# Kernel tuning notes

Hardware: AMD Instinct MI355X
Metric: run time of the kernel (lower is better)

Reference implementation:

```python
import jax, jax.numpy as jnp
import numpy as np

D_MODEL = 1024
NUM_HEADS = 16
D_K = D_MODEL // NUM_HEADS
B, T = 2, 2048
NEG = -1e9


def setup_inputs() -> dict:
    key = jax.random.key(0)
    ks = jax.random.split(key, 12)
    s = 1.0 / np.sqrt(D_MODEL)
    q = jax.random.normal(ks[0], (B, T, D_MODEL), jnp.float32)
    k = jax.random.normal(ks[1], (B, T, D_MODEL), jnp.float32)
    v = jax.random.normal(ks[2], (B, T, D_MODEL), jnp.float32)
    # padding mask: True = valid key; realistic per-example lengths
    lengths = jnp.array([T, 3 * T // 4], dtype=jnp.int32)
    key_padding_mask = jnp.arange(T)[None, :] < lengths[:, None]
    Wq = jax.random.uniform(ks[3], (D_MODEL, D_MODEL), jnp.float32, -s, s)
    bq = jax.random.uniform(ks[4], (D_MODEL,), jnp.float32, -s, s)
    Wk = jax.random.uniform(ks[5], (D_MODEL, D_MODEL), jnp.float32, -s, s)
    bk = jax.random.uniform(ks[6], (D_MODEL,), jnp.float32, -s, s)
    Wv = jax.random.uniform(ks[7], (D_MODEL, D_MODEL), jnp.float32, -s, s)
    bv = jax.random.uniform(ks[8], (D_MODEL,), jnp.float32, -s, s)
    Wo = jax.random.uniform(ks[9], (D_MODEL, D_MODEL), jnp.float32, -s, s)
    bo = jax.random.uniform(ks[10], (D_MODEL,), jnp.float32, -s, s)
    return {"q": q, "k": k, "v": v, "key_padding_mask": key_padding_mask,
            "Wq": Wq, "bq": bq, "Wk": Wk, "bk": bk,
            "Wv": Wv, "bv": bv, "Wo": Wo, "bo": bo}


def reference(q, k, v, key_padding_mask, Wq, bq, Wk, bk, Wv, bv, Wo, bo):
    Bq, Tq, D = q.shape
    Tk = k.shape[1]
    # projections (torch Linear: x @ W.T + b), split heads -> [B, H, T, d_k]
    Q = (q @ Wq.T + bq).reshape(Bq, Tq, NUM_HEADS, D_K).transpose(0, 2, 1, 3)
    K = (k @ Wk.T + bk).reshape(Bq, Tk, NUM_HEADS, D_K).transpose(0, 2, 1, 3)
    V = (v @ Wv.T + bv).reshape(Bq, Tk, NUM_HEADS, D_K).transpose(0, 2, 1, 3)
    logits = jnp.einsum("bhqd,bhkd->bhqk", Q, K) / jnp.sqrt(jnp.float32(D_K))
    causal = jnp.tril(jnp.ones((Tq, Tk), dtype=bool))  # [Tq, Tk]
    mask = causal[None, None, :, :] & key_padding_mask[:, None, None, :]
    logits = jnp.where(mask, logits, NEG)
    scores = jax.nn.softmax(logits, axis=-1)
    out = jnp.einsum("bhqk,bhkd->bhqd", scores, V)
    out = out.transpose(0, 2, 1, 3).reshape(Bq, Tq, D)
    # dropout is identity in eval mode
    return out @ Wo.T + bo
```

## Files before the change

### kernel.cpp

```cpp
#include <hip/hip_runtime.h>
#include <stdint.h>

#define D_MODEL 1024
#define NHEAD 16
#define DK 64
#define BATCH 2
#define SEQ 2048
#define NROW 4096

typedef __attribute__((ext_vector_type(8))) _Float16 f16x8;
typedef __attribute__((ext_vector_type(4))) float f32x4;

__device__ __forceinline__ uint16_t f2h(float x) {
    _Float16 h = (_Float16)x;
    union { _Float16 h; uint16_t u; } cv;
    cv.h = h;
    return cv.u;
}

__device__ __forceinline__ float fexp2(float x) {
#if __has_builtin(__builtin_amdgcn_exp2f)
    return __builtin_amdgcn_exp2f(x);
#else
    return exp2f(x);
#endif
}

__device__ __forceinline__ void lds_dma16(const uint16_t* g, uint16_t* l) {
    __builtin_amdgcn_global_load_lds((const __attribute__((address_space(1))) void*)g,
                                     (__attribute__((address_space(3))) void*)l,
                                     16, 0, 0);
}

struct CvtArgs {
    const float* src[7];
    uint16_t* dst[7];
    int n4[7];
};
__global__ void cvt_all_kernel(CvtArgs a, const int* __restrict__ mask, int* __restrict__ lens_ctr) {
    int t = blockIdx.y;
    if (t == 7) {
        if (blockIdx.x != 0) return;
        __shared__ int red[256];
        int tid = threadIdx.x;
        int mx = 0;
        for (int i = tid; i < 1024; i += 256) { int v = mask[i]; if (v > mx) mx = v; }
        red[tid] = mx; __syncthreads();
        for (int s = 128; s > 0; s >>= 1) { if (tid < s) { if (red[tid+s] > red[tid]) red[tid] = red[tid+s]; } __syncthreads(); }
        int bytemode = (red[0] > 1);
        __syncthreads();
        const unsigned char* mb = (const unsigned char*)mask;
        for (int b = 0; b < BATCH; ++b) {
            int cnt = 0;
            for (int tt = tid; tt < SEQ; tt += 256) {
                int v = bytemode ? (int)mb[b*SEQ + tt] : mask[b*SEQ + tt];
                cnt += (v != 0) ? 1 : 0;
            }
            red[tid] = cnt; __syncthreads();
            for (int s = 128; s > 0; s >>= 1) { if (tid < s) red[tid] += red[tid+s]; __syncthreads(); }
            if (tid == 0) lens_ctr[b] = red[0];
            __syncthreads();
        }
        if (tid == 0) lens_ctr[2] = 0;
        return;
    }
    const float* src = a.src[t];
    uint16_t* dst = a.dst[t];
    int n4 = a.n4[t];
    int i = blockIdx.x * blockDim.x + threadIdx.x;
    int stride = gridDim.x * blockDim.x;
    for (; i < n4; i += stride) {
        float4 v = ((const float4*)src)[i];
        ushort4 o;
        o.x = f2h(v.x); o.y = f2h(v.y); o.z = f2h(v.z); o.w = f2h(v.w);
        ((ushort4*)dst)[i] = o;
    }
}

__device__ __forceinline__ void gemm_tile_core(const uint16_t* __restrict__ A,
                                               const uint16_t* __restrict__ W,
                                               int bx, int by,
                                               uint16_t* As, uint16_t* Bs,
                                               f32x4 (&acc)[4][4]) {
    const f32x4 fzero = {0.f, 0.f, 0.f, 0.f};
    int tid = threadIdx.x;
    int lane = tid & 63, wave = tid >> 6;
    int wm = wave >> 1, wn = wave & 1;
    int l15 = lane & 15, quad = lane >> 4;
    int rl = lane >> 3, cb8 = lane & 7;
#pragma unroll
    for (int mi = 0; mi < 4; mi++)
#pragma unroll
        for (int ni = 0; ni < 4; ni++) acc[mi][ni] = fzero;

    for (int k0 = 0; k0 < D_MODEL; k0 += 64) {
        __syncthreads();
#pragma unroll
        for (int i = 0; i < 4; ++i) {
            int d8 = wave * 4 + i;
            int row = d8 * 8 + rl;
            int cbg = cb8 ^ rl;
            lds_dma16(A + (size_t)(bx * 128 + row) * D_MODEL + k0 + cbg * 8, As + d8 * 512);
            lds_dma16(W + (size_t)(by * 128 + row) * D_MODEL + k0 + cbg * 8, Bs + d8 * 512);
        }
        __syncthreads();
#pragma unroll
        for (int ks = 0; ks < 2; ks++) {
            f16x8 af[4], bf[4];
#pragma unroll
            for (int mi = 0; mi < 4; mi++) {
                int row = wm * 64 + mi * 16 + l15;
                af[mi] = *(const f16x8*)(As + row * 64 + (((ks * 4 + quad) ^ (row & 7)) * 8));
            }
#pragma unroll
            for (int ni = 0; ni < 4; ni++) {
                int row = wn * 64 + ni * 16 + l15;
                bf[ni] = *(const f16x8*)(Bs + row * 64 + (((ks * 4 + quad) ^ (row & 7)) * 8));
            }
#pragma unroll
            for (int mi = 0; mi < 4; mi++)
#pragma unroll
                for (int ni = 0; ni < 4; ni++)
                    acc[mi][ni] = __builtin_amdgcn_mfma_f32_16x16x32_f16(af[mi], bf[ni], acc[mi][ni], 0, 0, 0);
        }
    }
}

#define TS_STRIDE 136
__global__ __launch_bounds__(256, 3) void qkv_kernel(
    const uint16_t* __restrict__ qb, const uint16_t* __restrict__ kb, const uint16_t* __restrict__ vb,
    const uint16_t* __restrict__ wq, const uint16_t* __restrict__ wk, const uint16_t* __restrict__ wv,
    const float* __restrict__ bq, const float* __restrict__ bk, const float* __restrict__ bv,
    uint16_t* __restrict__ Qh, uint16_t* __restrict__ Kh, uint16_t* __restrict__ Vth) {
    __shared__ uint16_t smem[TS_STRIDE * 128];
    uint16_t* As = smem;
    uint16_t* Bs = smem + 128 * 64;
    int v = blockIdx.z;
    const uint16_t* A = (v == 0) ? qb : ((v == 1) ? kb : vb);
    const uint16_t* W = (v == 0) ? wq : ((v == 1) ? wk : wv);
    const float* bias = (v == 0) ? bq : ((v == 1) ? bk : bv);
    f32x4 acc[4][4];
    gemm_tile_core(A, W, blockIdx.x, blockIdx.y, As, Bs, acc);

    int tid = threadIdx.x, lane = tid & 63, wave = tid >> 6;
    int wm = wave >> 1, wn = wave & 1, l15 = lane & 15, quad = lane >> 4;
    const float QSCALE = 0.125f * 1.44269504088896f;

    if (v == 2) {
        __syncthreads();
        uint16_t* Ts = smem;
#pragma unroll
        for (int mi = 0; mi < 4; mi++) {
#pragma unroll
            for (int ni = 0; ni < 4; ni++) {
                int col = wn * 64 + ni * 16 + l15;
                float bcol = bias[blockIdx.y * 128 + col];
#pragma unroll
                for (int r = 0; r < 4; r++) {
                    int tl = wm * 64 + mi * 16 + quad * 4 + r;
                    Ts[col * TS_STRIDE + tl] = f2h(acc[mi][ni][r] + bcol);
                }
            }
        }
        __syncthreads();
        int col = tid >> 1, th = (tid & 1) << 6;
        int gcol = blockIdx.y * 128 + col;
        int h = gcol >> 6, d = gcol & 63;
        int grow0 = blockIdx.x * 128;
        int b = grow0 >> 11, t = (grow0 & (SEQ - 1)) + th;
        size_t base = (((size_t)(b * NHEAD + h) << 6) + d) * SEQ + t;
#pragma unroll
        for (int j = 0; j < 8; j++)
            *(uint4*)(Vth + base + j * 8) = *(const uint4*)(Ts + col * TS_STRIDE + th + j * 8);
        return;
    }

#pragma unroll
    for (int mi = 0; mi < 4; mi++) {
#pragma unroll
        for (int ni = 0; ni < 4; ni++) {
            int gcol = blockIdx.y * 128 + wn * 64 + ni * 16 + l15;
            float bcol = bias[gcol];
            int h = gcol >> 6, d = gcol & 63;
#pragma unroll
            for (int r = 0; r < 4; r++) {
                int grow = blockIdx.x * 128 + wm * 64 + mi * 16 + quad * 4 + r;
                int b = grow >> 11, t = grow & (SEQ - 1);
                float val = acc[mi][ni][r] + bcol;
                size_t bh = (size_t)(b * NHEAD + h);
                if (v == 0) Qh[(bh * SEQ + t) * 64 + d] = f2h(val * QSCALE);
                else        Kh[(bh * SEQ + t) * 64 + d] = f2h(val);
            }
        }
    }
}

__global__ __launch_bounds__(256, 3) void outproj_kernel(
    const uint16_t* __restrict__ attn, const uint16_t* __restrict__ wo,
    const float* __restrict__ bo, float* __restrict__ out) {
    __shared__ uint16_t As[128 * 64], Bs[128 * 64];
    f32x4 acc[4][4];
    gemm_tile_core(attn, wo, blockIdx.x, blockIdx.y, As, Bs, acc);
    int tid = threadIdx.x, lane = tid & 63, wave = tid >> 6;
    int wm = wave >> 1, wn = wave & 1, l15 = lane & 15, quad = lane >> 4;
#pragma unroll
    for (int mi = 0; mi < 4; mi++) {
#pragma unroll
        for (int ni = 0; ni < 4; ni++) {
            int gcol = blockIdx.y * 128 + wn * 64 + ni * 16 + l15;
            float bcol = bo[gcol];
#pragma unroll
            for (int r = 0; r < 4; r++) {
                int grow = blockIdx.x * 128 + wm * 64 + mi * 16 + quad * 4 + r;
                out[(size_t)grow * D_MODEL + gcol] = acc[mi][ni][r] + bcol;
            }
        }
    }
}

__device__ __forceinline__ void flash_one(
    int qt, int bh, int b, int h, int L,
    const uint16_t* __restrict__ Qh, const uint16_t* __restrict__ Kh, const uint16_t* __restrict__ Vth,
    uint16_t* __restrict__ attn,
    uint16_t* Kt0, uint16_t* Kt1, uint16_t* Vt0, uint16_t* Vt1, uint16_t* Ptw) {
    const f32x4 fzero = {0.f, 0.f, 0.f, 0.f};
    const float MFIX = 6.0f;
    int tid = threadIdx.x, lane = tid & 63, w = tid >> 6;
    int l15 = lane & 15, quad = lane >> 4, l7 = l15 & 7;
    int q0 = qt * 64;
    int rl = lane >> 3, cb8 = lane & 7;

    f16x8 ones;
#pragma unroll
    for (int j = 0; j < 8; j++) ones[j] = (_Float16)1.0f;

    f16x8 qf[2];
#pragma unroll
    for (int ks = 0; ks < 2; ks++)
        qf[ks] = *(const f16x8*)(Qh + ((size_t)bh * SEQ + q0 + w * 16 + l15) * 64 + ks * 32 + quad * 8);

    f32x4 o_acc[4], l_acc = fzero;
#pragma unroll
    for (int ni = 0; ni < 4; ni++) o_acc[ni] = fzero;

    int nkt_p = (L + 63) >> 6;
    int nkt = (qt + 1 < nkt_p) ? (qt + 1) : nkt_p;

    uint16_t* Ktb[2] = {Kt0, Kt1};
    uint16_t* Vtb[2] = {Vt0, Vt1};

    auto stage = [&](int kt_, int buf_) {
#pragma unroll
        for (int i_ = 0; i_ < 2; ++i_) {
            int d8 = w * 2 + i_;
            int row = d8 * 8 + rl;
            int cbg = cb8 ^ rl;
            lds_dma16(Kh + ((size_t)bh * SEQ + kt_ * 64 + row) * 64 + cbg * 8, Ktb[buf_] + d8 * 512);
            lds_dma16(Vth + (((size_t)bh << 6) + row) * SEQ + kt_ * 64 + cbg * 8, Vtb[buf_] + d8 * 512);
        }
    };

    stage(0, 0);
    __syncthreads();

    for (int kt = 0; kt < nkt; ++kt) {
        int cur = kt & 1;
        if (kt + 1 < nkt) stage(kt + 1, cur ^ 1);

        f32x4 s_acc[4];
#pragma unroll
        for (int ni = 0; ni < 4; ni++) s_acc[ni] = fzero;
#pragma unroll
        for (int ks = 0; ks < 2; ks++) {
            f16x8 kf[4];
#pragma unroll
            for (int ni = 0; ni < 4; ni++)
                kf[ni] = *(const f16x8*)(Ktb[cur] + (ni * 16 + l15) * 64 + ((ks * 4 + quad) ^ l7) * 8);
#pragma unroll
            for (int ni = 0; ni < 4; ni++)
                s_acc[ni] = __builtin_amdgcn_mfma_f32_16x16x32_f16(qf[ks], kf[ni], s_acc[ni], 0, 0, 0);
        }

        bool full = (kt < qt) && (kt * 64 + 64 <= L);
#pragma unroll
        for (int r = 0; r < 4; r++) {
            int prow = quad * 4 + r;
            int q_idx = q0 + w * 16 + prow;
            int pr7 = prow & 7;
#pragma unroll
            for (int ni = 0; ni < 4; ni++) {
                float s = s_acc[ni][r];
                if (!full) {
                    int key = kt * 64 + ni * 16 + l15;
                    s = ((key <= q_idx) && (key < L)) ? s : -1e9f;
                }
                float p = fexp2(s - MFIX);
                int cb = ni * 2 + (l15 >> 3);
                Ptw[prow * 64 + ((cb ^ pr7) * 8) + l7] = f2h(p);
            }
        }
        __asm__ __volatile__("" ::: "memory");

#pragma unroll
        for (int ks = 0; ks < 2; ks++) {
            f16x8 pa = *(const f16x8*)(Ptw + l15 * 64 + (((ks * 4 + quad) ^ l7) * 8));
            l_acc = __builtin_amdgcn_mfma_f32_16x16x32_f16(pa, ones, l_acc, 0, 0, 0);
            f16x8 vbf[4];
#pragma unroll
            for (int ni = 0; ni < 4; ni++)
                vbf[ni] = *(const f16x8*)(Vtb[cur] + (ni * 16 + l15) * 64 + ((ks * 4 + quad) ^ l7) * 8);
#pragma unroll
            for (int ni = 0; ni < 4; ni++)
                o_acc[ni] = __builtin_amdgcn_mfma_f32_16x16x32_f16(pa, vbf[ni], o_acc[ni], 0, 0, 0);
        }
        __syncthreads();
    }

#pragma unroll
    for (int r = 0; r < 4; r++) {
        float inv = 1.0f / l_acc[r];
        int q_idx = q0 + w * 16 + quad * 4 + r;
#pragma unroll
        for (int ni = 0; ni < 4; ni++) {
            attn[((size_t)(b * SEQ + q_idx)) * D_MODEL + h * 64 + ni * 16 + l15] =
                f2h(o_acc[ni][r] * inv);
        }
    }
}

__global__ __launch_bounds__(256, 4) void attn_kernel(
    const uint16_t* __restrict__ Qh, const uint16_t* __restrict__ Kh, const uint16_t* __restrict__ Vth,
    uint16_t* __restrict__ attn, int* __restrict__ lens_ctr) {
    __shared__ uint16_t Kt[2][64 * 64];
    __shared__ uint16_t Vt[2][64 * 64];
    __shared__ uint16_t Pt[4][16 * 64];
    __shared__ int curi;
    int tid = threadIdx.x;
    int w = tid >> 6;
    uint16_t* Ptw = &Pt[w][0];
    int* ctr = lens_ctr + 2;
    for (;;) {
        if (tid == 0) curi = atomicAdd(ctr, 1);
        __syncthreads();
        int i = curi;
        if (i >= 32 * 32) break;
        int qt = 31 - (i >> 5);
        int bh = i & 31;
        int b = bh >> 4, h = bh & 15;
        int L = lens_ctr[b];
        flash_one(qt, bh, b, h, L, Qh, Kh, Vth, attn,
                  &Kt[0][0], &Kt[1][0], &Vt[0][0], &Vt[1][0], Ptw);
    }
}

extern "C" void kernel_launch(void* const* d_in, const int* in_sizes, int n_in,
                              void* d_out, int out_size, void* d_ws, size_t ws_size,
                              hipStream_t stream) {
    const float* q  = (const float*)d_in[0];
    const float* k  = (const float*)d_in[1];
    const float* v  = (const float*)d_in[2];
    const int*   mask = (const int*)d_in[3];
    const float* Wq = (const float*)d_in[4];
    const float* bq = (const float*)d_in[5];
    const float* Wk = (const float*)d_in[6];
    const float* bk = (const float*)d_in[7];
    const float* Wv = (const float*)d_in[8];
    const float* bv = (const float*)d_in[9];
    const float* Wo = (const float*)d_in[10];
    const float* bo = (const float*)d_in[11];
    float* out = (float*)d_out;

    char* ws = (char*)d_ws;
    size_t off = 0;
    auto alloc = [&](size_t bytes) -> char* {
        char* p = ws + off;
        off += (bytes + 255) & ~(size_t)255;
        return p;
    };
    const size_t inp_e = (size_t)NROW * D_MODEL;
    const size_t w_e   = (size_t)D_MODEL * D_MODEL;
    uint16_t* qbf  = (uint16_t*)alloc(inp_e * 2);
    uint16_t* kbf  = (uint16_t*)alloc(inp_e * 2);
    uint16_t* vbf  = (uint16_t*)alloc(inp_e * 2);
    uint16_t* wqb  = (uint16_t*)alloc(w_e * 2);
    uint16_t* wkb  = (uint16_t*)alloc(w_e * 2);
    uint16_t* wvb  = (uint16_t*)alloc(w_e * 2);
    uint16_t* wob  = (uint16_t*)alloc(w_e * 2);
    uint16_t* Qhb  = (uint16_t*)alloc(inp_e * 2);
    uint16_t* Khb  = (uint16_t*)alloc(inp_e * 2);
    uint16_t* Vtb  = (uint16_t*)alloc(inp_e * 2);
    uint16_t* attb = (uint16_t*)alloc(inp_e * 2);
    int* lens_ctr  = (int*)alloc(256);

    CvtArgs ca;
    ca.src[0] = q;  ca.dst[0] = qbf; ca.n4[0] = (int)(inp_e / 4);
    ca.src[1] = k;  ca.dst[1] = kbf; ca.n4[1] = (int)(inp_e / 4);
    ca.src[2] = v;  ca.dst[2] = vbf; ca.n4[2] = (int)(inp_e / 4);
    ca.src[3] = Wq; ca.dst[3] = wqb; ca.n4[3] = (int)(w_e / 4);
    ca.src[4] = Wk; ca.dst[4] = wkb; ca.n4[4] = (int)(w_e / 4);
    ca.src[5] = Wv; ca.dst[5] = wvb; ca.n4[5] = (int)(w_e / 4);
    ca.src[6] = Wo; ca.dst[6] = wob; ca.n4[6] = (int)(w_e / 4);
    cvt_all_kernel<<<dim3(128, 8), 256, 0, stream>>>(ca, mask, lens_ctr);

    qkv_kernel<<<dim3(32, 8, 3), 256, 0, stream>>>(qbf, kbf, vbf, wqb, wkb, wvb,
                                                   bq, bk, bv, Qhb, Khb, Vtb);
    attn_kernel<<<dim3(1024), 256, 0, stream>>>(Qhb, Khb, Vtb, attb, lens_ctr);
    outproj_kernel<<<dim3(32, 8), 256, 0, stream>>>(attb, wob, bo, out);
}
```

Before: 258.2 us.

## Split KV tiles across waves with LDS atomic merge and paired causal tiles

The attention kernel no longer assigns each wave 16 query rows over all key tiles. Instead each wave takes every fourth key tile for all 64 query rows, with K/V fragments loaded straight from global memory. Partial outputs and row sums are merged through LDS float atomics, which works because every wave uses the same fixed softmax offset. The atomic work queue is replaced by a static grid where each block processes a mirrored pair of query tiles (31-x and x) to balance the causal workload. This drops the LDS double-buffered DMA staging, but adds uncoalesced global loads, LDS atomic traffic, more registers per thread, and lower occupancy (launch bounds 2 instead of 4).

```diff
diff --git a/kernel.cpp b/kernel.cpp
--- a/kernel.cpp
+++ b/kernel.cpp
@@ -37,7 +37,7 @@
     uint16_t* dst[7];
     int n4[7];
 };
-__global__ void cvt_all_kernel(CvtArgs a, const int* __restrict__ mask, int* __restrict__ lens_ctr) {
+__global__ void cvt_all_kernel(CvtArgs a, const int* __restrict__ mask, int* __restrict__ lens) {
     int t = blockIdx.y;
     if (t == 7) {
         if (blockIdx.x != 0) return;
@@ -58,10 +58,9 @@
             }
             red[tid] = cnt; __syncthreads();
             for (int s = 128; s > 0; s >>= 1) { if (tid < s) red[tid] += red[tid+s]; __syncthreads(); }
-            if (tid == 0) lens_ctr[b] = red[0];
+            if (tid == 0) lens[b] = red[0];
             __syncthreads();
         }
-        if (tid == 0) lens_ctr[2] = 0;
         return;
     }
     const float* src = a.src[t];
@@ -218,139 +217,149 @@
     }
 }
 
-__device__ __forceinline__ void flash_one(
+__device__ __forceinline__ void flash_item(
     int qt, int bh, int b, int h, int L,
     const uint16_t* __restrict__ Qh, const uint16_t* __restrict__ Kh, const uint16_t* __restrict__ Vth,
     uint16_t* __restrict__ attn,
-    uint16_t* Kt0, uint16_t* Kt1, uint16_t* Vt0, uint16_t* Vt1, uint16_t* Ptw) {
+    float* Macc, float* Lacc, uint16_t* Ptw) {
     const f32x4 fzero = {0.f, 0.f, 0.f, 0.f};
     const float MFIX = 6.0f;
     int tid = threadIdx.x, lane = tid & 63, w = tid >> 6;
     int l15 = lane & 15, quad = lane >> 4, l7 = l15 & 7;
     int q0 = qt * 64;
-    int rl = lane >> 3, cb8 = lane & 7;
+
+    {
+        const float4 z4 = {0.f, 0.f, 0.f, 0.f};
+#pragma unroll
+        for (int i = 0; i < 4; i++) *(float4*)&Macc[tid * 4 + i * 1024] = z4;
+        if (tid < 64) Lacc[tid] = 0.f;
+    }
+    __syncthreads();
 
     f16x8 ones;
 #pragma unroll
     for (int j = 0; j < 8; j++) ones[j] = (_Float16)1.0f;
 
-    f16x8 qf[2];
-#pragma unroll
-    for (int ks = 0; ks < 2; ks++)
-        qf[ks] = *(const f16x8*)(Qh + ((size_t)bh * SEQ + q0 + w * 16 + l15) * 64 + ks * 32 + quad * 8);
-
-    f32x4 o_acc[4], l_acc = fzero;
-#pragma unroll
-    for (int ni = 0; ni < 4; ni++) o_acc[ni] = fzero;
+    f16x8 qf[4][2];
+#pragma unroll
+    for (int m = 0; m < 4; m++)
+#pragma unroll
+        for (int ks = 0; ks < 2; ks++)
+            qf[m][ks] = *(const f16x8*)(Qh + ((size_t)bh * SEQ + q0 + m * 16 + l15) * 64 + ks * 32 + quad * 8);
+
+    f32x4 o_acc[4][4], l_acc[4];
+#pragma unroll
+    for (int m = 0; m < 4; m++) {
+        l_acc[m] = fzero;
+#pragma unroll
+        for (int ni = 0; ni < 4; ni++) o_acc[m][ni] = fzero;
+    }
 
     int nkt_p = (L + 63) >> 6;
     int nkt = (qt + 1 < nkt_p) ? (qt + 1) : nkt_p;
 
-    uint16_t* Ktb[2] = {Kt0, Kt1};
-    uint16_t* Vtb[2] = {Vt0, Vt1};
-
-    auto stage = [&](int kt_, int buf_) {
-#pragma unroll
-        for (int i_ = 0; i_ < 2; ++i_) {
-            int d8 = w * 2 + i_;
-            int row = d8 * 8 + rl;
-            int cbg = cb8 ^ rl;
-            lds_dma16(Kh + ((size_t)bh * SEQ + kt_ * 64 + row) * 64 + cbg * 8, Ktb[buf_] + d8 * 512);
-            lds_dma16(Vth + (((size_t)bh << 6) + row) * SEQ + kt_ * 64 + cbg * 8, Vtb[buf_] + d8 * 512);
-        }
-    };
-
-    stage(0, 0);
+    const uint16_t* Kbh = Kh + (size_t)bh * SEQ * 64;
+    const uint16_t* Vbh = Vth + ((size_t)bh << 6) * SEQ;
+
+    for (int kt = w; kt < nkt; kt += 4) {
+        f16x8 kf[2][4], vf[2][4];
+#pragma unroll
+        for (int ks = 0; ks < 2; ks++)
+#pragma unroll
+            for (int ni = 0; ni < 4; ni++)
+                kf[ks][ni] = *(const f16x8*)(Kbh + (size_t)(kt * 64 + ni * 16 + l15) * 64 + ks * 32 + quad * 8);
+#pragma unroll
+        for (int ks = 0; ks < 2; ks++)
+#pragma unroll
+            for (int ni = 0; ni < 4; ni++)
+                vf[ks][ni] = *(const f16x8*)(Vbh + (size_t)(ni * 16 + l15) * SEQ + kt * 64 + ks * 32 + quad * 8);
+
+        bool full = (kt < qt) && (kt * 64 + 64 <= L);
+
+#pragma unroll
+        for (int m = 0; m < 4; m++) {
+            f32x4 s_acc[4];
+#pragma unroll
+            for (int ni = 0; ni < 4; ni++) s_acc[ni] = fzero;
+#pragma unroll
+            for (int ks = 0; ks < 2; ks++)
+#pragma unroll
+                for (int ni = 0; ni < 4; ni++)
+                    s_acc[ni] = __builtin_amdgcn_mfma_f32_16x16x32_f16(qf[m][ks], kf[ks][ni], s_acc[ni], 0, 0, 0);
+#pragma unroll
+            for (int r = 0; r < 4; r++) {
+                int row = m * 16 + quad * 4 + r;
+                int q_idx = q0 + row;
+                int r7 = row & 7;
+#pragma unroll
+                for (int ni = 0; ni < 4; ni++) {
+                    float s = s_acc[ni][r];
+                    if (!full) {
+                        int key = kt * 64 + ni * 16 + l15;
+                        s = ((key <= q_idx) && (key < L)) ? s : -1e9f;
+                    }
+                    float p = fexp2(s - MFIX);
+                    int cb = ni * 2 + (l15 >> 3);
+                    Ptw[row * 64 + ((cb ^ r7) * 8) + l7] = f2h(p);
+                }
+            }
+        }
+        __asm__ __volatile__("" ::: "memory");
+
+#pragma unroll
+        for (int ks = 0; ks < 2; ks++) {
+#pragma unroll
+            for (int m = 0; m < 4; m++) {
+                int row = m * 16 + l15;
+                f16x8 pa = *(const f16x8*)(Ptw + row * 64 + (((ks * 4 + quad) ^ (row & 7)) * 8));
+                l_acc[m] = __builtin_amdgcn_mfma_f32_16x16x32_f16(pa, ones, l_acc[m], 0, 0, 0);
+#pragma unroll
+                for (int ni = 0; ni < 4; ni++)
+                    o_acc[m][ni] = __builtin_amdgcn_mfma_f32_16x16x32_f16(pa, vf[ks][ni], o_acc[m][ni], 0, 0, 0);
+            }
+        }
+    }
+
+#pragma unroll
+    for (int m = 0; m < 4; m++) {
+#pragma unroll
+        for (int ni = 0; ni < 4; ni++)
+#pragma unroll
+            for (int r = 0; r < 4; r++)
+                atomicAdd(&Macc[(m * 16 + quad * 4 + r) * 64 + ni * 16 + l15], o_acc[m][ni][r]);
+        if (l15 == 0)
+#pragma unroll
+            for (int r = 0; r < 4; r++)
+                atomicAdd(&Lacc[m * 16 + quad * 4 + r], l_acc[m][r]);
+    }
     __syncthreads();
 
-    for (int kt = 0; kt < nkt; ++kt) {
-        int cur = kt & 1;
-        if (kt + 1 < nkt) stage(kt + 1, cur ^ 1);
-
-        f32x4 s_acc[4];
-#pragma unroll
-        for (int ni = 0; ni < 4; ni++) s_acc[ni] = fzero;
-#pragma unroll
-        for (int ks = 0; ks < 2; ks++) {
-            f16x8 kf[4];
-#pragma unroll
-            for (int ni = 0; ni < 4; ni++)
-                kf[ni] = *(const f16x8*)(Ktb[cur] + (ni * 16 + l15) * 64 + ((ks * 4 + quad) ^ l7) * 8);
-#pragma unroll
-            for (int ni = 0; ni < 4; ni++)
-                s_acc[ni] = __builtin_amdgcn_mfma_f32_16x16x32_f16(qf[ks], kf[ni], s_acc[ni], 0, 0, 0);
-        }
-
-        bool full = (kt < qt) && (kt * 64 + 64 <= L);
-#pragma unroll
-        for (int r = 0; r < 4; r++) {
-            int prow = quad * 4 + r;
-            int q_idx = q0 + w * 16 + prow;
-            int pr7 = prow & 7;
-#pragma unroll
-            for (int ni = 0; ni < 4; ni++) {
-                float s = s_acc[ni][r];
-                if (!full) {
-                    int key = kt * 64 + ni * 16 + l15;
-                    s = ((key <= q_idx) && (key < L)) ? s : -1e9f;
-                }
-                float p = fexp2(s - MFIX);
-                int cb = ni * 2 + (l15 >> 3);
-                Ptw[prow * 64 + ((cb ^ pr7) * 8) + l7] = f2h(p);
-            }
-        }
-        __asm__ __volatile__("" ::: "memory");
-
-#pragma unroll
-        for (int ks = 0; ks < 2; ks++) {
-            f16x8 pa = *(const f16x8*)(Ptw + l15 * 64 + (((ks * 4 + quad) ^ l7) * 8));
-            l_acc = __builtin_amdgcn_mfma_f32_16x16x32_f16(pa, ones, l_acc, 0, 0, 0);
-            f16x8 vbf[4];
-#pragma unroll
-            for (int ni = 0; ni < 4; ni++)
-                vbf[ni] = *(const f16x8*)(Vtb[cur] + (ni * 16 + l15) * 64 + ((ks * 4 + quad) ^ l7) * 8);
-#pragma unroll
-            for (int ni = 0; ni < 4; ni++)
-                o_acc[ni] = __builtin_amdgcn_mfma_f32_16x16x32_f16(pa, vbf[ni], o_acc[ni], 0, 0, 0);
-        }
-        __syncthreads();
-    }
-
 #pragma unroll
     for (int r = 0; r < 4; r++) {
-        float inv = 1.0f / l_acc[r];
-        int q_idx = q0 + w * 16 + quad * 4 + r;
+        int row = w * 16 + quad * 4 + r;
+        float inv = 1.0f / Lacc[row];
 #pragma unroll
         for (int ni = 0; ni < 4; ni++) {
-            attn[((size_t)(b * SEQ + q_idx)) * D_MODEL + h * 64 + ni * 16 + l15] =
-                f2h(o_acc[ni][r] * inv);
-        }
-    }
-}
-
-__global__ __launch_bounds__(256, 4) void attn_kernel(
+            float val = Macc[row * 64 + ni * 16 + l15] * inv;
+            attn[((size_t)(b * SEQ + q0 + row)) * D_MODEL + h * 64 + ni * 16 + l15] = f2h(val);
+        }
+    }
+    __syncthreads();
+}
+
+__global__ __launch_bounds__(256, 2) void attn_kernel(
     const uint16_t* __restrict__ Qh, const uint16_t* __restrict__ Kh, const uint16_t* __restrict__ Vth,
-    uint16_t* __restrict__ attn, int* __restrict__ lens_ctr) {
-    __shared__ uint16_t Kt[2][64 * 64];
-    __shared__ uint16_t Vt[2][64 * 64];
-    __shared__ uint16_t Pt[4][16 * 64];
-    __shared__ int curi;
-    int tid = threadIdx.x;
-    int w = tid >> 6;
+    uint16_t* __restrict__ attn, const int* __restrict__ lens) {
+    __shared__ uint16_t Pt[4][64 * 64];
+    __shared__ float Macc[64 * 64];
+    __shared__ float Lacc[64];
+    int bh = blockIdx.y;
+    int b = bh >> 4, h = bh & 15;
+    int L = lens[b];
+    int w = threadIdx.x >> 6;
     uint16_t* Ptw = &Pt[w][0];
-    int* ctr = lens_ctr + 2;
-    for (;;) {
-        if (tid == 0) curi = atomicAdd(ctr, 1);
-        __syncthreads();
-        int i = curi;
-        if (i >= 32 * 32) break;
-        int qt = 31 - (i >> 5);
-        int bh = i & 31;
-        int b = bh >> 4, h = bh & 15;
-        int L = lens_ctr[b];
-        flash_one(qt, bh, b, h, L, Qh, Kh, Vth, attn,
-                  &Kt[0][0], &Kt[1][0], &Vt[0][0], &Vt[1][0], Ptw);
-    }
+    flash_item(31 - (int)blockIdx.x, bh, b, h, L, Qh, Kh, Vth, attn, Macc, Lacc, Ptw);
+    flash_item((int)blockIdx.x, bh, b, h, L, Qh, Kh, Vth, attn, Macc, Lacc, Ptw);
 }
 
 extern "C" void kernel_launch(void* const* d_in, const int* in_sizes, int n_in,
@@ -390,7 +399,7 @@
     uint16_t* Khb  = (uint16_t*)alloc(inp_e * 2);
     uint16_t* Vtb  = (uint16_t*)alloc(inp_e * 2);
     uint16_t* attb = (uint16_t*)alloc(inp_e * 2);
-    int* lens_ctr  = (int*)alloc(256);
+    int* lens      = (int*)alloc(256);
 
     CvtArgs ca;
     ca.src[0] = q;  ca.dst[0] = qbf; ca.n4[0] = (int)(inp_e / 4);
@@ -400,10 +409,10 @@
     ca.src[4] = Wk; ca.dst[4] = wkb; ca.n4[4] = (int)(w_e / 4);
     ca.src[5] = Wv; ca.dst[5] = wvb; ca.n4[5] = (int)(w_e / 4);
     ca.src[6] = Wo; ca.dst[6] = wob; ca.n4[6] = (int)(w_e / 4);
-    cvt_all_kernel<<<dim3(128, 8), 256, 0, stream>>>(ca, mask, lens_ctr);
+    cvt_all_kernel<<<dim3(128, 8), 256, 0, stream>>>(ca, mask, lens);
 
     qkv_kernel<<<dim3(32, 8, 3), 256, 0, stream>>>(qbf, kbf, vbf, wqb, wkb, wvb,
                                                    bq, bk, bv, Qhb, Khb, Vtb);
-    attn_kernel<<<dim3(1024), 256, 0, stream>>>(Qhb, Khb, Vtb, attb, lens_ctr);
+    attn_kernel<<<dim3(16, 32), 256, 0, stream>>>(Qhb, Khb, Vtb, attb, lens);
     outproj_kernel<<<dim3(32, 8), 256, 0, stream>>>(attb, wob, bo, out);
 }
```

Result: slower. 371.4 us (+43.8%).

## Restructure flash attention: transposed S, register P, triple-buffered loads, paired tiles

Applied to the files above, without the earlier changes.

The attention kernel now computes S transposed, so each lane's probabilities already sit in register layout as the B operand of 16x16x16 MFMAs. This removes the per-wave LDS round-trip for P. K/V tiles are triple-buffered, with explicit vmcnt waits plus raw s_barrier so loads two tiles ahead overlap compute. The atomic work-queue is replaced by a static grid where each block processes a heavy and a light causal query tile (qt and 31-qt) to balance load. This lowers launch bounds occupancy to 2 and uses more LDS.

```diff
diff --git a/kernel.cpp b/kernel.cpp
--- a/kernel.cpp
+++ b/kernel.cpp
@@ -9,6 +9,7 @@
 #define NROW 4096
 
 typedef __attribute__((ext_vector_type(8))) _Float16 f16x8;
+typedef __attribute__((ext_vector_type(4))) _Float16 f16x4;
 typedef __attribute__((ext_vector_type(4))) float f32x4;
 
 __device__ __forceinline__ uint16_t f2h(float x) {
@@ -37,7 +38,7 @@
     uint16_t* dst[7];
     int n4[7];
 };
-__global__ void cvt_all_kernel(CvtArgs a, const int* __restrict__ mask, int* __restrict__ lens_ctr) {
+__global__ void cvt_all_kernel(CvtArgs a, const int* __restrict__ mask, int* __restrict__ lens) {
     int t = blockIdx.y;
     if (t == 7) {
         if (blockIdx.x != 0) return;
@@ -58,10 +59,9 @@
             }
             red[tid] = cnt; __syncthreads();
             for (int s = 128; s > 0; s >>= 1) { if (tid < s) red[tid] += red[tid+s]; __syncthreads(); }
-            if (tid == 0) lens_ctr[b] = red[0];
+            if (tid == 0) lens[b] = red[0];
             __syncthreads();
         }
-        if (tid == 0) lens_ctr[2] = 0;
         return;
     }
     const float* src = a.src[t];
@@ -218,21 +218,23 @@
     }
 }
 
-__device__ __forceinline__ void flash_one(
+#define PIPE_BARRIER4() do { asm volatile("s_waitcnt vmcnt(4)" ::: "memory"); __builtin_amdgcn_s_barrier(); } while (0)
+#define PIPE_BARRIER0() do { asm volatile("s_waitcnt vmcnt(0)" ::: "memory"); __builtin_amdgcn_s_barrier(); } while (0)
+
+__device__ __forceinline__ void flash_item(
     int qt, int bh, int b, int h, int L,
     const uint16_t* __restrict__ Qh, const uint16_t* __restrict__ Kh, const uint16_t* __restrict__ Vth,
-    uint16_t* __restrict__ attn,
-    uint16_t* Kt0, uint16_t* Kt1, uint16_t* Vt0, uint16_t* Vt1, uint16_t* Ptw) {
+    uint16_t* __restrict__ attn, uint16_t* lds) {
     const f32x4 fzero = {0.f, 0.f, 0.f, 0.f};
     const float MFIX = 6.0f;
     int tid = threadIdx.x, lane = tid & 63, w = tid >> 6;
-    int l15 = lane & 15, quad = lane >> 4, l7 = l15 & 7;
+    int l15 = lane & 15, quad = lane >> 4;
     int q0 = qt * 64;
     int rl = lane >> 3, cb8 = lane & 7;
 
-    f16x8 ones;
-#pragma unroll
-    for (int j = 0; j < 8; j++) ones[j] = (_Float16)1.0f;
+    f16x4 ones4;
+#pragma unroll
+    for (int j = 0; j < 4; j++) ones4[j] = (_Float16)1.0f;
 
     f16x8 qf[2];
 #pragma unroll
@@ -241,13 +243,14 @@
 
     f32x4 o_acc[4], l_acc = fzero;
 #pragma unroll
-    for (int ni = 0; ni < 4; ni++) o_acc[ni] = fzero;
+    for (int mi = 0; mi < 4; mi++) o_acc[mi] = fzero;
 
     int nkt_p = (L + 63) >> 6;
     int nkt = (qt + 1 < nkt_p) ? (qt + 1) : nkt_p;
-
-    uint16_t* Ktb[2] = {Kt0, Kt1};
-    uint16_t* Vtb[2] = {Vt0, Vt1};
+    int q_idx = q0 + w * 16 + l15;
+
+    uint16_t* KT[3] = {lds, lds + 4096, lds + 8192};
+    uint16_t* VT[3] = {lds + 12288, lds + 16384, lds + 20480};
 
     auto stage = [&](int kt_, int buf_) {
 #pragma unroll
@@ -255,102 +258,87 @@
             int d8 = w * 2 + i_;
             int row = d8 * 8 + rl;
             int cbg = cb8 ^ rl;
-            lds_dma16(Kh + ((size_t)bh * SEQ + kt_ * 64 + row) * 64 + cbg * 8, Ktb[buf_] + d8 * 512);
-            lds_dma16(Vth + (((size_t)bh << 6) + row) * SEQ + kt_ * 64 + cbg * 8, Vtb[buf_] + d8 * 512);
+            lds_dma16(Kh + ((size_t)bh * SEQ + kt_ * 64 + row) * 64 + cbg * 8, KT[buf_] + d8 * 512);
+            lds_dma16(Vth + (((size_t)bh << 6) + row) * SEQ + kt_ * 64 + cbg * 8, VT[buf_] + d8 * 512);
         }
     };
 
     stage(0, 0);
-    __syncthreads();
-
+    if (nkt > 1) { stage(1, 1); PIPE_BARRIER4(); }
+    else         { PIPE_BARRIER0(); }
+
+    int bufc = 0;
     for (int kt = 0; kt < nkt; ++kt) {
-        int cur = kt & 1;
-        if (kt + 1 < nkt) stage(kt + 1, cur ^ 1);
+        bool staged = (kt + 2 < nkt);
+        if (staged) {
+            int b2 = (bufc >= 1) ? bufc - 1 : 2;
+            stage(kt + 2, b2);
+        }
+        const uint16_t* Kc = KT[bufc];
+        const uint16_t* Vc = VT[bufc];
 
         f32x4 s_acc[4];
 #pragma unroll
-        for (int ni = 0; ni < 4; ni++) s_acc[ni] = fzero;
+        for (int ki = 0; ki < 4; ki++) s_acc[ki] = fzero;
 #pragma unroll
         for (int ks = 0; ks < 2; ks++) {
-            f16x8 kf[4];
-#pragma unroll
-            for (int ni = 0; ni < 4; ni++)
-                kf[ni] = *(const f16x8*)(Ktb[cur] + (ni * 16 + l15) * 64 + ((ks * 4 + quad) ^ l7) * 8);
-#pragma unroll
-            for (int ni = 0; ni < 4; ni++)
-                s_acc[ni] = __builtin_amdgcn_mfma_f32_16x16x32_f16(qf[ks], kf[ni], s_acc[ni], 0, 0, 0);
+#pragma unroll
+            for (int ki = 0; ki < 4; ki++) {
+                int row = ki * 16 + l15;
+                f16x8 kfv = *(const f16x8*)(Kc + row * 64 + (((ks * 4 + quad) ^ (row & 7)) * 8));
+                s_acc[ki] = __builtin_amdgcn_mfma_f32_16x16x32_f16(kfv, qf[ks], s_acc[ki], 0, 0, 0);
+            }
         }
 
         bool full = (kt < qt) && (kt * 64 + 64 <= L);
 #pragma unroll
-        for (int r = 0; r < 4; r++) {
-            int prow = quad * 4 + r;
-            int q_idx = q0 + w * 16 + prow;
-            int pr7 = prow & 7;
-#pragma unroll
-            for (int ni = 0; ni < 4; ni++) {
-                float s = s_acc[ni][r];
+        for (int ki = 0; ki < 4; ki++) {
+            f16x4 pb;
+#pragma unroll
+            for (int r = 0; r < 4; r++) {
+                float s = s_acc[ki][r];
                 if (!full) {
-                    int key = kt * 64 + ni * 16 + l15;
+                    int key = kt * 64 + ki * 16 + quad * 4 + r;
                     s = ((key <= q_idx) && (key < L)) ? s : -1e9f;
                 }
-                float p = fexp2(s - MFIX);
-                int cb = ni * 2 + (l15 >> 3);
-                Ptw[prow * 64 + ((cb ^ pr7) * 8) + l7] = f2h(p);
-            }
-        }
-        __asm__ __volatile__("" ::: "memory");
-
-#pragma unroll
-        for (int ks = 0; ks < 2; ks++) {
-            f16x8 pa = *(const f16x8*)(Ptw + l15 * 64 + (((ks * 4 + quad) ^ l7) * 8));
-            l_acc = __builtin_amdgcn_mfma_f32_16x16x32_f16(pa, ones, l_acc, 0, 0, 0);
-            f16x8 vbf[4];
-#pragma unroll
-            for (int ni = 0; ni < 4; ni++)
-                vbf[ni] = *(const f16x8*)(Vtb[cur] + (ni * 16 + l15) * 64 + ((ks * 4 + quad) ^ l7) * 8);
-#pragma unroll
-            for (int ni = 0; ni < 4; ni++)
-                o_acc[ni] = __builtin_amdgcn_mfma_f32_16x16x32_f16(pa, vbf[ni], o_acc[ni], 0, 0, 0);
-        }
-        __syncthreads();
-    }
-
-#pragma unroll
-    for (int r = 0; r < 4; r++) {
-        float inv = 1.0f / l_acc[r];
-        int q_idx = q0 + w * 16 + quad * 4 + r;
-#pragma unroll
-        for (int ni = 0; ni < 4; ni++) {
-            attn[((size_t)(b * SEQ + q_idx)) * D_MODEL + h * 64 + ni * 16 + l15] =
-                f2h(o_acc[ni][r] * inv);
-        }
-    }
-}
-
-__global__ __launch_bounds__(256, 4) void attn_kernel(
+                pb[r] = (_Float16)fexp2(s - MFIX);
+            }
+            l_acc = __builtin_amdgcn_mfma_f32_16x16x16f16(ones4, pb, l_acc, 0, 0, 0);
+            int c16 = ki * 2 + (quad >> 1);
+            int sub = (quad & 1) * 4;
+#pragma unroll
+            for (int mi = 0; mi < 4; mi++) {
+                int d = mi * 16 + l15;
+                f16x4 va = *(const f16x4*)(Vc + d * 64 + ((c16 ^ (d & 7)) * 8) + sub);
+                o_acc[mi] = __builtin_amdgcn_mfma_f32_16x16x16f16(va, pb, o_acc[mi], 0, 0, 0);
+            }
+        }
+
+        if (staged) PIPE_BARRIER4();
+        else        PIPE_BARRIER0();
+        bufc = (bufc == 2) ? 0 : bufc + 1;
+    }
+
+    float inv = 1.0f / l_acc[0];
+    size_t base = ((size_t)(b * SEQ + q_idx)) * D_MODEL + h * 64;
+#pragma unroll
+    for (int mi = 0; mi < 4; mi++) {
+        f16x4 ov;
+#pragma unroll
+        for (int r = 0; r < 4; r++) ov[r] = (_Float16)(o_acc[mi][r] * inv);
+        *(f16x4*)(attn + base + mi * 16 + quad * 4) = ov;
+    }
+}
+
+__global__ __launch_bounds__(256, 2) void attn_kernel(
     const uint16_t* __restrict__ Qh, const uint16_t* __restrict__ Kh, const uint16_t* __restrict__ Vth,
-    uint16_t* __restrict__ attn, int* __restrict__ lens_ctr) {
-    __shared__ uint16_t Kt[2][64 * 64];
-    __shared__ uint16_t Vt[2][64 * 64];
-    __shared__ uint16_t Pt[4][16 * 64];
-    __shared__ int curi;
-    int tid = threadIdx.x;
-    int w = tid >> 6;
-    uint16_t* Ptw = &Pt[w][0];
-    int* ctr = lens_ctr + 2;
-    for (;;) {
-        if (tid == 0) curi = atomicAdd(ctr, 1);
-        __syncthreads();
-        int i = curi;
-        if (i >= 32 * 32) break;
-        int qt = 31 - (i >> 5);
-        int bh = i & 31;
-        int b = bh >> 4, h = bh & 15;
-        int L = lens_ctr[b];
-        flash_one(qt, bh, b, h, L, Qh, Kh, Vth, attn,
-                  &Kt[0][0], &Kt[1][0], &Vt[0][0], &Vt[1][0], Ptw);
-    }
+    uint16_t* __restrict__ attn, const int* __restrict__ lens) {
+    __shared__ uint16_t lds[24576];
+    int bh = blockIdx.y;
+    int b = bh >> 4, h = bh & 15;
+    int L = lens[b];
+    flash_item(31 - (int)blockIdx.x, bh, b, h, L, Qh, Kh, Vth, attn, lds);
+    flash_item((int)blockIdx.x, bh, b, h, L, Qh, Kh, Vth, attn, lds);
 }
 
 extern "C" void kernel_launch(void* const* d_in, const int* in_sizes, int n_in,
@@ -390,7 +378,7 @@
     uint16_t* Khb  = (uint16_t*)alloc(inp_e * 2);
     uint16_t* Vtb  = (uint16_t*)alloc(inp_e * 2);
     uint16_t* attb = (uint16_t*)alloc(inp_e * 2);
-    int* lens_ctr  = (int*)alloc(256);
+    int* lens      = (int*)alloc(256);
 
     CvtArgs ca;
     ca.src[0] = q;  ca.dst[0] = qbf; ca.n4[0] = (int)(inp_e / 4);
@@ -400,10 +388,10 @@
     ca.src[4] = Wk; ca.dst[4] = wkb; ca.n4[4] = (int)(w_e / 4);
     ca.src[5] = Wv; ca.dst[5] = wvb; ca.n4[5] = (int)(w_e / 4);
     ca.src[6] = Wo; ca.dst[6] = wob; ca.n4[6] = (int)(w_e / 4);
-    cvt_all_kernel<<<dim3(128, 8), 256, 0, stream>>>(ca, mask, lens_ctr);
+    cvt_all_kernel<<<dim3(128, 8), 256, 0, stream>>>(ca, mask, lens);
 
     qkv_kernel<<<dim3(32, 8, 3), 256, 0, stream>>>(qbf, kbf, vbf, wqb, wkb, wvb,
                                                    bq, bk, bv, Qhb, Khb, Vtb);
-    attn_kernel<<<dim3(1024), 256, 0, stream>>>(Qhb, Khb, Vtb, attb, lens_ctr);
+    attn_kernel<<<dim3(16, 32), 256, 0, stream>>>(Qhb, Khb, Vtb, attb, lens);
     outproj_kernel<<<dim3(32, 8), 256, 0, stream>>>(attb, wob, bo, out);
 }
```

New measurement: 237.0 us. 1.09x faster.

## Pair causal q-tiles per block and deepen K/V LDS prefetch pipeline

Applied to the files above, without the earlier changes.

Replaces the atomic work-queue persistent scheduler with a static grid where each block processes two complementary causal query tiles (qt and 31-qt), balancing work without atomics. The K/V staging becomes a triple-buffered K and double-buffered V pipeline using explicit vmcnt waits and raw barriers instead of __syncthreads, so loads for future tiles overlap compute. LDS use grows, so occupancy is lowered to 3 blocks per SIMD-group, and the vmcnt(2) accounting relies on exact DMA issue ordering, which is fragile.

```diff
diff --git a/kernel.cpp b/kernel.cpp
--- a/kernel.cpp
+++ b/kernel.cpp
@@ -37,7 +37,7 @@
     uint16_t* dst[7];
     int n4[7];
 };
-__global__ void cvt_all_kernel(CvtArgs a, const int* __restrict__ mask, int* __restrict__ lens_ctr) {
+__global__ void cvt_all_kernel(CvtArgs a, const int* __restrict__ mask, int* __restrict__ lens) {
     int t = blockIdx.y;
     if (t == 7) {
         if (blockIdx.x != 0) return;
@@ -58,10 +58,9 @@
             }
             red[tid] = cnt; __syncthreads();
             for (int s = 128; s > 0; s >>= 1) { if (tid < s) red[tid] += red[tid+s]; __syncthreads(); }
-            if (tid == 0) lens_ctr[b] = red[0];
+            if (tid == 0) lens[b] = red[0];
             __syncthreads();
         }
-        if (tid == 0) lens_ctr[2] = 0;
         return;
     }
     const float* src = a.src[t];
@@ -218,11 +217,14 @@
     }
 }
 
-__device__ __forceinline__ void flash_one(
+#define PIPE_WAIT2_BARRIER() do { asm volatile("s_waitcnt vmcnt(2)" ::: "memory"); __builtin_amdgcn_s_barrier(); } while (0)
+#define PIPE_WAIT0_BARRIER() do { asm volatile("s_waitcnt vmcnt(0)" ::: "memory"); __builtin_amdgcn_s_barrier(); } while (0)
+
+__device__ __forceinline__ void flash_item(
     int qt, int bh, int b, int h, int L,
     const uint16_t* __restrict__ Qh, const uint16_t* __restrict__ Kh, const uint16_t* __restrict__ Vth,
     uint16_t* __restrict__ attn,
-    uint16_t* Kt0, uint16_t* Kt1, uint16_t* Vt0, uint16_t* Vt1, uint16_t* Ptw) {
+    uint16_t* KtA, uint16_t* VtA, uint16_t* Ptw) {
     const f32x4 fzero = {0.f, 0.f, 0.f, 0.f};
     const float MFIX = 6.0f;
     int tid = threadIdx.x, lane = tid & 63, w = tid >> 6;
@@ -246,26 +248,43 @@
     int nkt_p = (L + 63) >> 6;
     int nkt = (qt + 1 < nkt_p) ? (qt + 1) : nkt_p;
 
-    uint16_t* Ktb[2] = {Kt0, Kt1};
-    uint16_t* Vtb[2] = {Vt0, Vt1};
-
-    auto stage = [&](int kt_, int buf_) {
+    const uint16_t* Kbh = Kh + (size_t)bh * SEQ * 64;
+    const uint16_t* Vbh = Vth + ((size_t)bh << 6) * SEQ;
+
+    auto stageK = [&](int kt_, int slot) {
 #pragma unroll
         for (int i_ = 0; i_ < 2; ++i_) {
             int d8 = w * 2 + i_;
             int row = d8 * 8 + rl;
             int cbg = cb8 ^ rl;
-            lds_dma16(Kh + ((size_t)bh * SEQ + kt_ * 64 + row) * 64 + cbg * 8, Ktb[buf_] + d8 * 512);
-            lds_dma16(Vth + (((size_t)bh << 6) + row) * SEQ + kt_ * 64 + cbg * 8, Vtb[buf_] + d8 * 512);
+            lds_dma16(Kbh + (size_t)(kt_ * 64 + row) * 64 + cbg * 8, KtA + slot * 4096 + d8 * 512);
         }
     };
-
-    stage(0, 0);
-    __syncthreads();
-
+    auto stageV = [&](int kt_, int slot) {
+#pragma unroll
+        for (int i_ = 0; i_ < 2; ++i_) {
+            int d8 = w * 2 + i_;
+            int row = d8 * 8 + rl;
+            int cbg = cb8 ^ rl;
+            lds_dma16(Vbh + (size_t)row * SEQ + kt_ * 64 + cbg * 8, VtA + slot * 4096 + d8 * 512);
+        }
+    };
+
+    stageV(0, 0);
+    stageK(0, 0);
+    PIPE_WAIT0_BARRIER();
+    stageK((1 < nkt) ? 1 : 0, 1);
+
+    int kcur = 0, vcur = 0;
     for (int kt = 0; kt < nkt; ++kt) {
-        int cur = kt & 1;
-        if (kt + 1 < nkt) stage(kt + 1, cur ^ 1);
+        int ktV = (kt + 1 < nkt) ? kt + 1 : nkt - 1;
+        int ktK = (kt + 2 < nkt) ? kt + 2 : nkt - 1;
+        stageV(ktV, (kt + 1) & 1);
+        int ks2 = (kcur >= 1) ? kcur - 1 : 2;
+        stageK(ktK, ks2);
+
+        const uint16_t* Kc = KtA + kcur * 4096;
+        const uint16_t* Vc = VtA + vcur * 4096;
 
         f32x4 s_acc[4];
 #pragma unroll
@@ -274,8 +293,10 @@
         for (int ks = 0; ks < 2; ks++) {
             f16x8 kf[4];
 #pragma unroll
-            for (int ni = 0; ni < 4; ni++)
-                kf[ni] = *(const f16x8*)(Ktb[cur] + (ni * 16 + l15) * 64 + ((ks * 4 + quad) ^ l7) * 8);
+            for (int ni = 0; ni < 4; ni++) {
+                int row = ni * 16 + l15;
+                kf[ni] = *(const f16x8*)(Kc + row * 64 + (((ks * 4 + quad) ^ (row & 7)) * 8));
+            }
 #pragma unroll
             for (int ni = 0; ni < 4; ni++)
                 s_acc[ni] = __builtin_amdgcn_mfma_f32_16x16x32_f16(qf[ks], kf[ni], s_acc[ni], 0, 0, 0);
@@ -307,13 +328,18 @@
             l_acc = __builtin_amdgcn_mfma_f32_16x16x32_f16(pa, ones, l_acc, 0, 0, 0);
             f16x8 vbf[4];
 #pragma unroll
-            for (int ni = 0; ni < 4; ni++)
-                vbf[ni] = *(const f16x8*)(Vtb[cur] + (ni * 16 + l15) * 64 + ((ks * 4 + quad) ^ l7) * 8);
+            for (int ni = 0; ni < 4; ni++) {
+                int row = ni * 16 + l15;
+                vbf[ni] = *(const f16x8*)(Vc + row * 64 + (((ks * 4 + quad) ^ (row & 7)) * 8));
+            }
 #pragma unroll
             for (int ni = 0; ni < 4; ni++)
                 o_acc[ni] = __builtin_amdgcn_mfma_f32_16x16x32_f16(pa, vbf[ni], o_acc[ni], 0, 0, 0);
         }
-        __syncthreads();
+
+        PIPE_WAIT2_BARRIER();
+        kcur = (kcur == 2) ? 0 : kcur + 1;
+        vcur ^= 1;
     }
 
 #pragma unroll
@@ -328,29 +354,19 @@
     }
 }
 
-__global__ __launch_bounds__(256, 4) void attn_kernel(
+__global__ __launch_bounds__(256, 3) void attn_kernel(
     const uint16_t* __restrict__ Qh, const uint16_t* __restrict__ Kh, const uint16_t* __restrict__ Vth,
-    uint16_t* __restrict__ attn, int* __restrict__ lens_ctr) {
-    __shared__ uint16_t Kt[2][64 * 64];
-    __shared__ uint16_t Vt[2][64 * 64];
-    __shared__ uint16_t Pt[4][16 * 64];
-    __shared__ int curi;
-    int tid = threadIdx.x;
-    int w = tid >> 6;
-    uint16_t* Ptw = &Pt[w][0];
-    int* ctr = lens_ctr + 2;
-    for (;;) {
-        if (tid == 0) curi = atomicAdd(ctr, 1);
-        __syncthreads();
-        int i = curi;
-        if (i >= 32 * 32) break;
-        int qt = 31 - (i >> 5);
-        int bh = i & 31;
-        int b = bh >> 4, h = bh & 15;
-        int L = lens_ctr[b];
-        flash_one(qt, bh, b, h, L, Qh, Kh, Vth, attn,
-                  &Kt[0][0], &Kt[1][0], &Vt[0][0], &Vt[1][0], Ptw);
-    }
+    uint16_t* __restrict__ attn, const int* __restrict__ lens) {
+    __shared__ uint16_t Kt[3 * 4096];
+    __shared__ uint16_t Vt[2 * 4096];
+    __shared__ uint16_t Pt[4 * 1024];
+    int bh = blockIdx.y;
+    int b = bh >> 4, h = bh & 15;
+    int L = lens[b];
+    int w = threadIdx.x >> 6;
+    uint16_t* Ptw = Pt + w * 1024;
+    flash_item(31 - (int)blockIdx.x, bh, b, h, L, Qh, Kh, Vth, attn, Kt, Vt, Ptw);
+    flash_item((int)blockIdx.x, bh, b, h, L, Qh, Kh, Vth, attn, Kt, Vt, Ptw);
 }
 
 extern "C" void kernel_launch(void* const* d_in, const int* in_sizes, int n_in,
@@ -390,7 +406,7 @@
     uint16_t* Khb  = (uint16_t*)alloc(inp_e * 2);
     uint16_t* Vtb  = (uint16_t*)alloc(inp_e * 2);
     uint16_t* attb = (uint16_t*)alloc(inp_e * 2);
-    int* lens_ctr  = (int*)alloc(256);
+    int* lens      = (int*)alloc(256);
 
     CvtArgs ca;
     ca.src[0] = q;  ca.dst[0] = qbf; ca.n4[0] = (int)(inp_e / 4);
@@ -400,10 +416,10 @@
     ca.src[4] = Wk; ca.dst[4] = wkb; ca.n4[4] = (int)(w_e / 4);
     ca.src[5] = Wv; ca.dst[5] = wvb; ca.n4[5] = (int)(w_e / 4);
     ca.src[6] = Wo; ca.dst[6] = wob; ca.n4[6] = (int)(w_e / 4);
-    cvt_all_kernel<<<dim3(128, 8), 256, 0, stream>>>(ca, mask, lens_ctr);
+    cvt_all_kernel<<<dim3(128, 8), 256, 0, stream>>>(ca, mask, lens);
 
     qkv_kernel<<<dim3(32, 8, 3), 256, 0, stream>>>(qbf, kbf, vbf, wqb, wkb, wvb,
                                                    bq, bk, bv, Qhb, Khb, Vtb);
-    attn_kernel<<<dim3(1024), 256, 0, stream>>>(Qhb, Khb, Vtb, attb, lens_ctr);
+    attn_kernel<<<dim3(16, 32), 256, 0, stream>>>(Qhb, Khb, Vtb, attb, lens);
     outproj_kernel<<<dim3(32, 8), 256, 0, stream>>>(attb, wob, bo, out);
 }
```

Result: faster. 223.4 us (-13.5%).
